# Optimization experiments

Measured on AMD Instinct MI355X. Metric: run time of the kernel, lower is better.

The kernel has to match this reference:

```python
import jax, jax.numpy as jnp
import numpy as np

B, N, DEG = 64, 512, 16        # graphs, nodes per graph, avg degree
C, HID = 10, 128               # input feat dim (== num_classes quirk), hidden
E = B * N * DEG                # total edges (fixed; pooling masks edges)


def _gcn(x, W, b, src, dst, emask, n):
    # PyG GCNConv: add self-loops, symmetric norm D^-1/2 (A+I) D^-1/2 (XW) + b
    h = x @ W
    deg = jax.ops.segment_sum(emask, dst, num_segments=n) + 1.0  # +1 self-loop
    dinv = jax.lax.rsqrt(deg)
    norm = dinv[src] * dinv[dst] * emask
    agg = jax.ops.segment_sum(h[src] * norm[:, None], dst, num_segments=n)
    return agg + h * (dinv * dinv)[:, None] + b  # self-loop term + bias


def _sag_pool(x, src, dst, emask, Wp, bp, n_per):
    # SAGPooling: score = tanh(GCN(x)); per-graph top-k (ratio=0.5); x' = x[perm]*score
    n = x.shape[0]
    score = jnp.tanh(_gcn(x, Wp, bp, src, dst, emask, n)[:, 0])
    k = n_per // 2
    vals, idx = jax.lax.top_k(score.reshape(B, n_per), k)  # [B,k]
    perm = (idx + (jnp.arange(B) * n_per)[:, None]).reshape(-1)
    xk = x[perm] * vals.reshape(-1)[:, None]
    # relabel edges; drop edges touching removed nodes via mask (fixed E)
    mapping = jnp.full((n,), -1, jnp.int32).at[perm].set(
        jnp.arange(B * k, dtype=jnp.int32))
    ns, nd = mapping[src], mapping[dst]
    nmask = emask * ((ns >= 0) & (nd >= 0)).astype(emask.dtype)
    return xk, jnp.maximum(ns, 0), jnp.maximum(nd, 0), nmask, k


def _readout(x, k):
    # global max pool || global mean pool (all kept nodes are real, no padding)
    xg = x.reshape(B, k, -1)
    return jnp.concatenate([xg.max(axis=1), xg.mean(axis=1)], axis=1)


def setup_inputs() -> dict:
    key = jax.random.key(0)
    ks = jax.random.split(key, 16)
    x = jax.random.normal(ks[0], (B * N, C), jnp.float32)
    off = jnp.repeat(jnp.arange(B, dtype=jnp.int32) * N, N * DEG)
    src = jax.random.randint(ks[1], (E,), 0, N, jnp.int32) + off
    dst = jax.random.randint(ks[2], (E,), 0, N, jnp.int32) + off
    p = lambda k, s: jax.random.normal(k, s, jnp.float32) * 0.05
    return {
        "x": x, "src": src, "dst": dst,
        "W1": p(ks[3], (C, HID)), "b1": jnp.zeros((HID,), jnp.float32),
        "W2": p(ks[4], (HID, HID)), "b2": jnp.zeros((HID,), jnp.float32),
        "W3": p(ks[5], (HID, HID)), "b3": jnp.zeros((HID,), jnp.float32),
        "Wp": p(ks[6], (HID, 1)), "bp": jnp.zeros((1,), jnp.float32),
        "L1W": p(ks[7], (2 * HID, HID)), "L1b": jnp.zeros((HID,), jnp.float32),
        "L2W": p(ks[8], (HID, HID // 2)), "L2b": jnp.zeros((HID // 2,), jnp.float32),
    }


def reference(x, src, dst, W1, b1, W2, b2, W3, b3, Wp, bp, L1W, L1b, L2W, L2b):
    emask = jnp.ones((E,), jnp.float32)
    h = jax.nn.relu(_gcn(x, W1, b1, src, dst, emask, B * N))
    h, src, dst, emask, k = _sag_pool(h, src, dst, emask, Wp, bp, N)
    x1 = _readout(h, k)
    h = jax.nn.relu(_gcn(h, W2, b2, src, dst, emask, B * k))
    h, src, dst, emask, k = _sag_pool(h, src, dst, emask, Wp, bp, k)
    x2 = _readout(h, k)
    h = jax.nn.relu(_gcn(h, W3, b3, src, dst, emask, B * k))
    h, src, dst, emask, k = _sag_pool(h, src, dst, emask, Wp, bp, k)
    x3 = _readout(h, k)
    z = x1 + x2 + x3
    z = jax.nn.relu(z @ L1W + L1b)
    # dropout inactive in eval mode
    z = jax.nn.relu(z @ L2W + L2b)
    return jax.nn.log_softmax(z, axis=1)
```

## Files before the change

### kernel.cpp

```cpp
#include <hip/hip_runtime.h>
#include <math.h>

#define BGR 64
#define N0 512
#define E_TOT (BGR*N0*16)
#define EPG 8192
#define HID 128
#define LOFF2 32768
#define LOFF3 49152

#define HSW(r,l) (((r)<<3) | (((l)+(r))&7))

__device__ __forceinline__ void bitonic_sort(float* sv, int* si, float v, int idx,
                                             int t, int nper, bool act){
  for (int kk = 2; kk <= nper; kk <<= 1){
    for (int jj = kk >> 1; jj > 0; jj >>= 1){
      if (jj >= 64){
        if (act){ sv[t] = v; si[t] = idx; }
        __syncthreads();
        if (act){
          int p = t ^ jj;
          float pv = sv[p]; int pi = si[p];
          bool amLower = (t & jj) == 0;
          bool dirDesc = (t & kk) == 0;
          bool betterMine = (v > pv) || (v == pv && idx < pi);
          if ((amLower == dirDesc) != betterMine){ v = pv; idx = pi; }
        }
        __syncthreads();
      } else if (act){
        float pv = __shfl_xor(v, jj);
        int   pi = __shfl_xor(idx, jj);
        bool amLower = (t & jj) == 0;
        bool dirDesc = (t & kk) == 0;
        bool betterMine = (v > pv) || (v == pv && idx < pi);
        if ((amLower == dirDesc) != betterMine){ v = pv; idx = pi; }
      }
    }
  }
  if (act){ sv[t] = v; si[t] = idx; }
  __syncthreads();
}

__device__ __forceinline__ void relabel_pre(
    int2* __restrict__ edges, int2* __restrict__ csr, const int* si,
    int* map_, int* sb, int* cur, float* dl, int* wsum,
    int* __restrict__ rowptr, int* __restrict__ cnt, float* __restrict__ dinv,
    const int2* epre,
    int t, int nper, int k, int gbase, int gbnew, int ebase, int loff){
  if (t < nper) map_[t] = -1;
  if (t < k) sb[t] = 0;
  __syncthreads();
  if (t < k) map_[si[t]] = t;
  __syncthreads();
  int2 ebuf[8];
  #pragma unroll
  for (int it = 0; it < 8; it++){
    int2 e = epre[it];
    int2 ne = make_int2(-1, 0);
    if (e.x >= 0){
      int ns = map_[e.x - gbase], nd = map_[e.y - gbase];
      if (ns >= 0 && nd >= 0){
        ne = make_int2(gbnew + ns, gbnew + nd);
        atomicAdd(&sb[nd], 1);
      }
    }
    ebuf[it] = ne;
    edges[ebase + it*1024 + t] = ne;
  }
  __syncthreads();
  int vdeg = (t < k) ? sb[t] : 0;
  int lane = t & 63, wid = t >> 6;
  int x = vdeg;
  #pragma unroll
  for (int off = 1; off < 64; off <<= 1){
    int y = __shfl_up(x, off);
    if (lane >= off) x += y;
  }
  if (t < k && lane == 63) wsum[wid] = x;
  __syncthreads();
  if (t < k){
    int prefix = 0;
    #pragma unroll
    for (int wj = 0; wj < 4; wj++) prefix += (wj < wid) ? wsum[wj] : 0;
    int excl = x + prefix - vdeg;
    rowptr[loff + gbnew + t] = ebase + excl;
    cnt[loff + gbnew + t] = vdeg;
    cur[t] = excl;
    float dv = rsqrtf((float)vdeg + 1.f);
    dl[t] = dv;
    dinv[loff + gbnew + t] = dv;
  }
  __syncthreads();
  #pragma unroll
  for (int it = 0; it < 8; it++){
    int2 e = ebuf[it];
    if (e.x >= 0){
      int sl = e.x - gbnew, dc = e.y - gbnew;
      int pos = atomicAdd(&cur[dc], 1);
      csr[ebase + pos] = make_int2(e.x, __float_as_int(dl[sl]*dl[dc]));
    }
  }
  __syncthreads();
}

__global__ __launch_bounds__(1024) void k_topo0(
    const int* __restrict__ s0, const int* __restrict__ d0,
    int2* __restrict__ edges, int* __restrict__ cnt, int* __restrict__ rowptr,
    float* __restrict__ dinv, int2* __restrict__ csr){
  __shared__ int   deg[512];
  __shared__ int   cur[512];
  __shared__ float dl[512];
  __shared__ int   wsum[8];
  int g = (blockIdx.x & 7)*8 + (blockIdx.x >> 3);
  int t = threadIdx.x;
  int gbase = g*N0, ebase = g*EPG;
  if (t < 512) deg[t] = 0;
  __syncthreads();
  int2 ebuf[8];
  #pragma unroll
  for (int it = 0; it < 8; it++){
    int i = ebase + it*1024 + t;
    int2 e = make_int2(s0[i], d0[i]);
    ebuf[it] = e;
    edges[i] = e;
    atomicAdd(&deg[e.y - gbase], 1);
  }
  __syncthreads();
  int vdeg = (t < 512) ? deg[t] : 0;
  int lane = t & 63, wid = t >> 6;
  int x = vdeg;
  #pragma unroll
  for (int off = 1; off < 64; off <<= 1){
    int y = __shfl_up(x, off);
    if (lane >= off) x += y;
  }
  if (t < 512 && lane == 63) wsum[wid] = x;
  __syncthreads();
  if (t < 512){
    int prefix = 0;
    #pragma unroll
    for (int wj = 0; wj < 8; wj++) prefix += (wj < wid) ? wsum[wj] : 0;
    int excl = x + prefix - vdeg;
    rowptr[gbase + t] = ebase + excl;
    cnt[gbase + t] = vdeg;
    cur[t] = excl;
    float dv = rsqrtf((float)vdeg + 1.f);
    dl[t] = dv;
    dinv[gbase + t] = dv;
  }
  __syncthreads();
  #pragma unroll
  for (int it = 0; it < 8; it++){
    int2 e = ebuf[it];
    int sl = e.x - gbase, dc = e.y - gbase;
    int pos = atomicAdd(&cur[dc], 1);
    csr[ebase + pos] = make_int2(e.x, __float_as_int(dl[sl]*dl[dc]));
  }
}

__global__ __launch_bounds__(512) void k_l1_fused(
    const float* __restrict__ x, const float* __restrict__ W1,
    const int2* __restrict__ csr, const int* __restrict__ rowptr,
    const int* __restrict__ cnt, const float* __restrict__ dinv,
    const float* __restrict__ b1, const float* __restrict__ Wp,
    float4* __restrict__ gout4, float* __restrict__ hp_part){
  extern __shared__ float hl[];
  int b = blockIdx.x;
  int xcd = b & 7, idx = b >> 3;
  int graph = xcd*8 + (idx >> 3);
  int sub = idx & 7;
  int qf = sub >> 1, half = sub & 1;
  int t = threadIdx.x;
  int gbase = graph*N0;
  int fp = t & 31;
  int f = qf*32 + fp;
  float wcol[10];
  #pragma unroll
  for (int k = 0; k < 10; k++) wcol[k] = W1[k*HID + f];
  for (int n = t >> 5; n < N0; n += 16){
    const float* xr = x + (gbase + n)*10;
    float acc = 0.f;
    #pragma unroll
    for (int k = 0; k < 10; k++) acc += xr[k]*wcol[k];
    hl[n*32 + ((((fp>>2)+n)&7)<<2) + (fp&3)] = acc;
  }
  __syncthreads();
  const float4* hl4 = (const float4*)hl;
  int l = t & 7, grp = t >> 3;
  float4 bb = ((const float4*)b1)[qf*8 + l];
  float4 wp = ((const float4*)Wp)[qf*8 + l];
  int n0 = half*256;
  for (int nl = n0 + grp; nl < n0 + 256; nl += 64){
    int node = gbase + nl;
    int start = rowptr[node], c = cnt[node];
    float4 acc = make_float4(0.f,0.f,0.f,0.f);
    int j = 0;
    for (; j + 4 <= c; j += 4){
      int2 e0 = csr[start+j],   e1 = csr[start+j+1];
      int2 e2 = csr[start+j+2], e3 = csr[start+j+3];
      float4 h0 = hl4[HSW(e0.x - gbase, l)];
      float4 h1 = hl4[HSW(e1.x - gbase, l)];
      float4 h2 = hl4[HSW(e2.x - gbase, l)];
      float4 h3 = hl4[HSW(e3.x - gbase, l)];
      float w0 = __int_as_float(e0.y), w1 = __int_as_float(e1.y);
      float w2 = __int_as_float(e2.y), w3 = __int_as_float(e3.y);
      acc.x += w0*h0.x + w1*h1.x + w2*h2.x + w3*h3.x;
      acc.y += w0*h0.y + w1*h1.y + w2*h2.y + w3*h3.y;
      acc.z += w0*h0.z + w1*h1.z + w2*h2.z + w3*h3.z;
      acc.w += w0*h0.w + w1*h1.w + w2*h2.w + w3*h3.w;
    }
    for (; j < c; j++){
      int2 e = csr[start + j];
      float wgt = __int_as_float(e.y);
      float4 hv = hl4[HSW(e.x - gbase, l)];
      acc.x += wgt*hv.x; acc.y += wgt*hv.y; acc.z += wgt*hv.z; acc.w += wgt*hv.w;
    }
    float di = dinv[node], dd = di*di;
    float4 hs = hl4[HSW(nl, l)];
    float4 v;
    v.x = fmaxf(acc.x + hs.x*dd + bb.x, 0.f);
    v.y = fmaxf(acc.y + hs.y*dd + bb.y, 0.f);
    v.z = fmaxf(acc.z + hs.z*dd + bb.z, 0.f);
    v.w = fmaxf(acc.w + hs.w*dd + bb.w, 0.f);
    gout4[node*32 + qf*8 + l] = v;
    float contrib = v.x*wp.x + v.y*wp.y + v.z*wp.z + v.w*wp.w;
    #pragma unroll
    for (int off = 4; off; off >>= 1) contrib += __shfl_down(contrib, off, 8);
    if (l == 0) hp_part[qf*32768 + node] = contrib;
  }
}

__global__ __launch_bounds__(1024) void k_mega1(
    const float4* __restrict__ gout4, const float* __restrict__ hppt,
    int2* __restrict__ csr, int* __restrict__ rowptr, int* __restrict__ cnt,
    float* __restrict__ dinv, const float* __restrict__ bp,
    int2* __restrict__ edges, int* __restrict__ sig, float* __restrict__ svg,
    float* __restrict__ z){
  __shared__ float sv[512];
  __shared__ int   si[512];
  __shared__ float hpl[512];
  __shared__ union UA {
    float spart[1024];
    struct { float4 pmx[32][32]; float4 psm[32][32]; } ro;
    struct { int map_[512]; int sb[512]; int cur[256]; } rl;
  } u;
  __shared__ float dl[256];
  __shared__ int   wsum[4];
  int g = (blockIdx.x & 7)*8 + (blockIdx.x >> 3);
  int t = threadIdx.x;
  int gbase = g*N0, ebase = g*EPG, gb2 = g*256;
  float bp0 = bp[0];
  int2 epre[8];
  #pragma unroll
  for (int it = 0; it < 8; it++) epre[it] = edges[ebase + it*1024 + t];
  if (t < 512){
    int node = gbase + t;
    hpl[t] = hppt[node] + hppt[32768+node] + hppt[65536+node] + hppt[98304+node];
  }
  __syncthreads();
  {
    int n = t & 511, p = t >> 9;
    int start = rowptr[gbase + n], c = cnt[gbase + n];
    int lo = (c*p) >> 1, hi = (c*(p+1)) >> 1;
    float a = 0.f;
    for (int j = lo; j < hi; j++){
      int2 e = csr[start + j];
      a += __int_as_float(e.y)*hpl[e.x - gbase];
    }
    u.spart[t] = a;
  }
  __syncthreads();
  float v = 0.f; int idx = t;
  if (t < 512){
    float a = u.spart[t] + u.spart[t + 512];
    float di = dinv[gbase + t];
    v = tanhf(a + hpl[t]*di*di + bp0);
  }
  __syncthreads();
  bitonic_sort(sv, si, v, idx, t, 512, t < 512);
  if (t < 256){ sig[g*512 + t] = si[t]; svg[g*512 + t] = sv[t]; }
  int l = t & 31, j0 = t >> 5;
  {
    float4 mx = make_float4(-INFINITY,-INFINITY,-INFINITY,-INFINITY);
    float4 sm = make_float4(0.f,0.f,0.f,0.f);
    for (int j = j0; j < 256; j += 32){
      float val = sv[j]; int row = si[j];
      float4 hv = gout4[(gbase + row)*32 + l];
      float4 o = make_float4(hv.x*val, hv.y*val, hv.z*val, hv.w*val);
      mx.x = fmaxf(mx.x, o.x); mx.y = fmaxf(mx.y, o.y);
      mx.z = fmaxf(mx.z, o.z); mx.w = fmaxf(mx.w, o.w);
      sm.x += o.x; sm.y += o.y; sm.z += o.z; sm.w += o.w;
    }
    u.ro.pmx[j0][l] = mx; u.ro.psm[j0][l] = sm;
  }
  __syncthreads();
  if (t < 32){
    float4 M = u.ro.pmx[0][t], S = u.ro.psm[0][t];
    #pragma unroll
    for (int q = 1; q < 32; q++){
      float4 m2 = u.ro.pmx[q][t], s2 = u.ro.psm[q][t];
      M.x = fmaxf(M.x, m2.x); M.y = fmaxf(M.y, m2.y);
      M.z = fmaxf(M.z, m2.z); M.w = fmaxf(M.w, m2.w);
      S.x += s2.x; S.y += s2.y; S.z += s2.z; S.w += s2.w;
    }
    float ki = 1.f/256.f;
    float* zp = z + g*256;
    zp[t*4+0] = M.x; zp[t*4+1] = M.y; zp[t*4+2] = M.z; zp[t*4+3] = M.w;
    zp[128+t*4+0] = S.x*ki; zp[128+t*4+1] = S.y*ki;
    zp[128+t*4+2] = S.z*ki; zp[128+t*4+3] = S.w*ki;
  }
  __syncthreads();
  relabel_pre(edges, csr, si, u.rl.map_, u.rl.sb, u.rl.cur, dl, wsum,
              rowptr, cnt, dinv, epre, t, 512, 256, gbase, gb2, ebase, LOFF2);
}

__global__ __launch_bounds__(512) void k_lvl2(
    const float4* __restrict__ gout4,
    const int* __restrict__ sig, const float* __restrict__ svg,
    const float* __restrict__ W2, const float* __restrict__ b2,
    const float* __restrict__ Wp,
    const int2* __restrict__ csr, const int* __restrict__ rowptr,
    const int* __restrict__ cnt, const float* __restrict__ dinv,
    float4* __restrict__ g2out4, float* __restrict__ hp2p){
  __shared__ float hL[256*32];
  int b = blockIdx.x;
  int jb = b & 63, s8 = b >> 6;
  int s = s8 >> 1, half = s8 & 1;
  int g = (jb & 7)*8 + (jb >> 3);
  int t = threadIdx.x;
  int gbase = g*N0, gb2 = g*256;
  float4* hL4 = (float4*)hL;
  {
    int f4 = t & 7, rg = t >> 3;
    int rbase = rg*4;
    const float* Wb = W2 + s*32 + f4*4;
    int ri[4]; float rv[4];
    #pragma unroll
    for (int q = 0; q < 4; q++){
      ri[q] = sig[g*512 + rbase + q];
      rv[q] = svg[g*512 + rbase + q];
    }
    float4 acc[4];
    #pragma unroll
    for (int q = 0; q < 4; q++) acc[q] = make_float4(0.f,0.f,0.f,0.f);
    for (int i = 0; i < HID; i += 4){
      float4 w0 = *(const float4*)(Wb + (i+0)*HID);
      float4 w1 = *(const float4*)(Wb + (i+1)*HID);
      float4 w2 = *(const float4*)(Wb + (i+2)*HID);
      float4 w3 = *(const float4*)(Wb + (i+3)*HID);
      #pragma unroll
      for (int q = 0; q < 4; q++){
        float4 xv = gout4[(gbase + ri[q])*32 + (i>>2)];
        float vx = xv.x*rv[q], vy = xv.y*rv[q], vz = xv.z*rv[q], vw = xv.w*rv[q];
        acc[q].x += vx*w0.x + vy*w1.x + vz*w2.x + vw*w3.x;
        acc[q].y += vx*w0.y + vy*w1.y + vz*w2.y + vw*w3.y;
        acc[q].z += vx*w0.z + vy*w1.z + vz*w2.z + vw*w3.z;
        acc[q].w += vx*w0.w + vy*w1.w + vz*w2.w + vw*w3.w;
      }
    }
    #pragma unroll
    for (int q = 0; q < 4; q++) hL4[HSW(rbase+q, f4)] = acc[q];
  }
  __syncthreads();
  int l = t & 7, grpn = t >> 3;
  float4 bb = ((const float4*)b2)[s*8 + l];
  float4 wp = ((const float4*)Wp)[s*8 + l];
  for (int it = 0; it < 2; it++){
    int n = half*128 + it*64 + grpn;
    int node = gb2 + n;
    int start = rowptr[LOFF2 + node], c = cnt[LOFF2 + node];
    float4 acc = make_float4(0.f,0.f,0.f,0.f);
    int j = 0;
    for (; j + 4 <= c; j += 4){
      int2 e0 = csr[start+j],   e1 = csr[start+j+1];
      int2 e2 = csr[start+j+2], e3 = csr[start+j+3];
      float4 h0 = hL4[HSW(e0.x - gb2, l)];
      float4 h1 = hL4[HSW(e1.x - gb2, l)];
      float4 h2 = hL4[HSW(e2.x - gb2, l)];
      float4 h3 = hL4[HSW(e3.x - gb2, l)];
      float w0 = __int_as_float(e0.y), w1 = __int_as_float(e1.y);
      float w2 = __int_as_float(e2.y), w3 = __int_as_float(e3.y);
      acc.x += w0*h0.x + w1*h1.x + w2*h2.x + w3*h3.x;
      acc.y += w0*h0.y + w1*h1.y + w2*h2.y + w3*h3.y;
      acc.z += w0*h0.z + w1*h1.z + w2*h2.z + w3*h3.z;
      acc.w += w0*h0.w + w1*h1.w + w2*h2.w + w3*h3.w;
    }
    for (; j < c; j++){
      int2 e = csr[start + j];
      float wgt = __int_as_float(e.y);
      float4 hv = hL4[HSW(e.x - gb2, l)];
      acc.x += wgt*hv.x; acc.y += wgt*hv.y; acc.z += wgt*hv.z; acc.w += wgt*hv.w;
    }
    float di = dinv[LOFF2 + node], dd = di*di;
    float4 hs = hL4[HSW(n, l)];
    float4 v;
    v.x = fmaxf(acc.x + hs.x*dd + bb.x, 0.f);
    v.y = fmaxf(acc.y + hs.y*dd + bb.y, 0.f);
    v.z = fmaxf(acc.z + hs.z*dd + bb.z, 0.f);
    v.w = fmaxf(acc.w + hs.w*dd + bb.w, 0.f);
    g2out4[node*32 + s*8 + l] = v;
    float contrib = v.x*wp.x + v.y*wp.y + v.z*wp.z + v.w*wp.w;
    #pragma unroll
    for (int off = 4; off; off >>= 1) contrib += __shfl_down(contrib, off, 8);
    if (l == 0) hp2p[s*16384 + node] = contrib;
  }
}

__global__ __launch_bounds__(1024) void k_mega2(
    const float4* __restrict__ g2out4, const float* __restrict__ hp2p,
    int2* __restrict__ csr, int* __restrict__ rowptr, int* __restrict__ cnt,
    float* __restrict__ dinv, const float* __restrict__ bp,
    int2* __restrict__ edges, int* __restrict__ sig, float* __restrict__ svg,
    float* __restrict__ z){
  __shared__ float sv[256];
  __shared__ int   si[256];
  __shared__ float hpl[256];
  __shared__ union UB {
    float spart[1024];
    struct { float4 pmx[32][32]; float4 psm[32][32]; } ro;
    struct { int map_[256]; int sb[128]; int cur[128]; } rl;
  } u;
  __shared__ float dl[128];
  __shared__ int   wsum[4];
  int g = (blockIdx.x & 7)*8 + (blockIdx.x >> 3);
  int t = threadIdx.x;
  int gb2 = g*256, gb3 = g*128, ebase = g*EPG;
  float bp0 = bp[0];
  int2 epre[8];
  #pragma unroll
  for (int it = 0; it < 8; it++) epre[it] = edges[ebase + it*1024 + t];
  if (t < 256){
    int node = gb2 + t;
    hpl[t] = hp2p[node] + hp2p[16384+node] + hp2p[32768+node] + hp2p[49152+node];
  }
  __syncthreads();
  {
    int n = t & 255, p = t >> 8;
    int start = rowptr[LOFF2 + gb2 + n], c = cnt[LOFF2 + gb2 + n];
    int lo = (c*p) >> 2, hi = (c*(p+1)) >> 2;
    float a = 0.f;
    for (int j = lo; j < hi; j++){
      int2 e = csr[start + j];
      a += __int_as_float(e.y)*hpl[e.x - gb2];
    }
    u.spart[t] = a;
  }
  __syncthreads();
  float v = 0.f; int idx = t;
  if (t < 256){
    float a = u.spart[t] + u.spart[t+256] + u.spart[t+512] + u.spart[t+768];
    float di = dinv[LOFF2 + gb2 + t];
    v = tanhf(a + hpl[t]*di*di + bp0);
  }
  __syncthreads();
  bitonic_sort(sv, si, v, idx, t, 256, t < 256);
  if (t < 128){ sig[g*512 + t] = si[t]; svg[g*512 + t] = sv[t]; }
  int l = t & 31, j0 = t >> 5;
  {
    float4 mx = make_float4(-INFINITY,-INFINITY,-INFINITY,-INFINITY);
    float4 sm = make_float4(0.f,0.f,0.f,0.f);
    for (int j = j0; j < 128; j += 32){
      float val = sv[j]; int row = si[j];
      float4 hv = g2out4[(gb2 + row)*32 + l];
      float4 o = make_float4(hv.x*val, hv.y*val, hv.z*val, hv.w*val);
      mx.x = fmaxf(mx.x, o.x); mx.y = fmaxf(mx.y, o.y);
      mx.z = fmaxf(mx.z, o.z); mx.w = fmaxf(mx.w, o.w);
      sm.x += o.x; sm.y += o.y; sm.z += o.z; sm.w += o.w;
    }
    u.ro.pmx[j0][l] = mx; u.ro.psm[j0][l] = sm;
  }
  __syncthreads();
  if (t < 32){
    float4 M = u.ro.pmx[0][t], S = u.ro.psm[0][t];
    #pragma unroll
    for (int q = 1; q < 32; q++){
      float4 m2 = u.ro.pmx[q][t], s2 = u.ro.psm[q][t];
      M.x = fmaxf(M.x, m2.x); M.y = fmaxf(M.y, m2.y);
      M.z = fmaxf(M.z, m2.z); M.w = fmaxf(M.w, m2.w);
      S.x += s2.x; S.y += s2.y; S.z += s2.z; S.w += s2.w;
    }
    float ki = 1.f/128.f;
    float* zp = z + g*256;
    zp[t*4+0] += M.x; zp[t*4+1] += M.y; zp[t*4+2] += M.z; zp[t*4+3] += M.w;
    zp[128+t*4+0] += S.x*ki; zp[128+t*4+1] += S.y*ki;
    zp[128+t*4+2] += S.z*ki; zp[128+t*4+3] += S.w*ki;
  }
  __syncthreads();
  relabel_pre(edges, csr, si, u.rl.map_, u.rl.sb, u.rl.cur, dl, wsum,
              rowptr, cnt, dinv, epre, t, 256, 128, gb2, gb3, ebase, LOFF3);
}

__global__ __launch_bounds__(512) void k_lvl3(
    const float4* __restrict__ g2out4,
    const int* __restrict__ sig, const float* __restrict__ svg,
    const float* __restrict__ W3, const float* __restrict__ b3,
    const float* __restrict__ Wp,
    const int2* __restrict__ csr, const int* __restrict__ rowptr,
    const int* __restrict__ cnt, const float* __restrict__ dinv,
    float4* __restrict__ g3out4, float* __restrict__ hp3p){
  __shared__ float hL[128*32];
  int b = blockIdx.x;
  int jb = b & 63, s8 = b >> 6;
  int s = s8 >> 1, half = s8 & 1;
  int g = (jb & 7)*8 + (jb >> 3);
  int t = threadIdx.x;
  int gb2 = g*256, gb3 = g*128;
  float4* hL4 = (float4*)hL;
  {
    int f4 = t & 7, rg = t >> 3;
    int rbase = rg*2;
    const float* Wb = W3 + s*32 + f4*4;
    int ri[2]; float rv[2];
    #pragma unroll
    for (int q = 0; q < 2; q++){
      ri[q] = sig[g*512 + rbase + q];
      rv[q] = svg[g*512 + rbase + q];
    }
    float4 acc[2];
    #pragma unroll
    for (int q = 0; q < 2; q++) acc[q] = make_float4(0.f,0.f,0.f,0.f);
    for (int i = 0; i < HID; i += 4){
      float4 w0 = *(const float4*)(Wb + (i+0)*HID);
      float4 w1 = *(const float4*)(Wb + (i+1)*HID);
      float4 w2 = *(const float4*)(Wb + (i+2)*HID);
      float4 w3 = *(const float4*)(Wb + (i+3)*HID);
      #pragma unroll
      for (int q = 0; q < 2; q++){
        float4 xv = g2out4[(gb2 + ri[q])*32 + (i>>2)];
        float vx = xv.x*rv[q], vy = xv.y*rv[q], vz = xv.z*rv[q], vw = xv.w*rv[q];
        acc[q].x += vx*w0.x + vy*w1.x + vz*w2.x + vw*w3.x;
        acc[q].y += vx*w0.y + vy*w1.y + vz*w2.y + vw*w3.y;
        acc[q].z += vx*w0.z + vy*w1.z + vz*w2.z + vw*w3.z;
        acc[q].w += vx*w0.w + vy*w1.w + vz*w2.w + vw*w3.w;
      }
    }
    #pragma unroll
    for (int q = 0; q < 2; q++) hL4[HSW(rbase+q, f4)] = acc[q];
  }
  __syncthreads();
  int l = t & 7, grpn = t >> 3;
  float4 bb = ((const float4*)b3)[s*8 + l];
  float4 wp = ((const float4*)Wp)[s*8 + l];
  {
    int n = half*64 + grpn;
    int node = gb3 + n;
    int start = rowptr[LOFF3 + node], c = cnt[LOFF3 + node];
    float4 acc = make_float4(0.f,0.f,0.f,0.f);
    int j = 0;
    for (; j + 4 <= c; j += 4){
      int2 e0 = csr[start+j],   e1 = csr[start+j+1];
      int2 e2 = csr[start+j+2], e3 = csr[start+j+3];
      float4 h0 = hL4[HSW(e0.x - gb3, l)];
      float4 h1 = hL4[HSW(e1.x - gb3, l)];
      float4 h2 = hL4[HSW(e2.x - gb3, l)];
      float4 h3 = hL4[HSW(e3.x - gb3, l)];
      float w0 = __int_as_float(e0.y), w1 = __int_as_float(e1.y);
      float w2 = __int_as_float(e2.y), w3 = __int_as_float(e3.y);
      acc.x += w0*h0.x + w1*h1.x + w2*h2.x + w3*h3.x;
      acc.y += w0*h0.y + w1*h1.y + w2*h2.y + w3*h3.y;
      acc.z += w0*h0.z + w1*h1.z + w2*h2.z + w3*h3.z;
      acc.w += w0*h0.w + w1*h1.w + w2*h2.w + w3*h3.w;
    }
    for (; j < c; j++){
      int2 e = csr[start + j];
      float wgt = __int_as_float(e.y);
      float4 hv = hL4[HSW(e.x - gb3, l)];
      acc.x += wgt*hv.x; acc.y += wgt*hv.y; acc.z += wgt*hv.z; acc.w += wgt*hv.w;
    }
    float di = dinv[LOFF3 + node], dd = di*di;
    float4 hs = hL4[HSW(n, l)];
    float4 v;
    v.x = fmaxf(acc.x + hs.x*dd + bb.x, 0.f);
    v.y = fmaxf(acc.y + hs.y*dd + bb.y, 0.f);
    v.z = fmaxf(acc.z + hs.z*dd + bb.z, 0.f);
    v.w = fmaxf(acc.w + hs.w*dd + bb.w, 0.f);
    g3out4[node*32 + s*8 + l] = v;
    float contrib = v.x*wp.x + v.y*wp.y + v.z*wp.z + v.w*wp.w;
    #pragma unroll
    for (int off = 4; off; off >>= 1) contrib += __shfl_down(contrib, off, 8);
    if (l == 0) hp3p[s*8192 + node] = contrib;
  }
}

__global__ __launch_bounds__(1024) void k_mega3(
    const float4* __restrict__ g3out4, const float* __restrict__ hp3p,
    const int2* __restrict__ csr, const int* __restrict__ rowptr,
    const int* __restrict__ cnt, const float* __restrict__ dinv,
    const float* __restrict__ bp, float* __restrict__ z,
    const float* __restrict__ L1W, const float* __restrict__ L1b,
    const float* __restrict__ L2W, const float* __restrict__ L2b,
    float* __restrict__ out){
  __shared__ float sv[128];
  __shared__ int   si[128];
  __shared__ float hpl[128];
  __shared__ union UC {
    float spart[1024];
    struct { float4 pmx[32][32]; float4 psm[32][32]; } ro;
  } u;
  __shared__ float zr[256];
  __shared__ float h1l[128];
  __shared__ float h2l[64];
  __shared__ float red[2];
  int g = (blockIdx.x & 7)*8 + (blockIdx.x >> 3);
  int t = threadIdx.x;
  int gb3 = g*128;
  float bp0 = bp[0];
  if (t < 128){
    int node = gb3 + t;
    hpl[t] = hp3p[node] + hp3p[8192+node] + hp3p[16384+node] + hp3p[24576+node];
  }
  __syncthreads();
  {
    int n = t & 127, p = t >> 7;
    int start = rowptr[LOFF3 + gb3 + n], c = cnt[LOFF3 + gb3 + n];
    int lo = (c*p) >> 3, hi = (c*(p+1)) >> 3;
    float a = 0.f;
    for (int j = lo; j < hi; j++){
      int2 e = csr[start + j];
      a += __int_as_float(e.y)*hpl[e.x - gb3];
    }
    u.spart[t] = a;
  }
  __syncthreads();
  float v = 0.f; int idx = t;
  if (t < 128){
    float a = 0.f;
    #pragma unroll
    for (int pp = 0; pp < 8; pp++) a += u.spart[t + pp*128];
    float di = dinv[LOFF3 + gb3 + t];
    v = tanhf(a + hpl[t]*di*di + bp0);
  }
  __syncthreads();
  bitonic_sort(sv, si, v, idx, t, 128, t < 128);
  int l = t & 31, j0 = t >> 5;
  {
    float4 mx = make_float4(-INFINITY,-INFINITY,-INFINITY,-INFINITY);
    float4 sm = make_float4(0.f,0.f,0.f,0.f);
    for (int j = j0; j < 64; j += 32){
      float val = sv[j]; int row = si[j];
      float4 hv = g3out4[(gb3 + row)*32 + l];
      float4 o = make_float4(hv.x*val, hv.y*val, hv.z*val, hv.w*val);
      mx.x = fmaxf(mx.x, o.x); mx.y = fmaxf(mx.y, o.y);
      mx.z = fmaxf(mx.z, o.z); mx.w = fmaxf(mx.w, o.w);
      sm.x += o.x; sm.y += o.y; sm.z += o.z; sm.w += o.w;
    }
    u.ro.pmx[j0][l] = mx; u.ro.psm[j0][l] = sm;
  }
  __syncthreads();
  if (t < 32){
    float4 M = u.ro.pmx[0][t], S = u.ro.psm[0][t];
    #pragma unroll
    for (int q = 1; q < 32; q++){
      float4 m2 = u.ro.pmx[q][t], s2 = u.ro.psm[q][t];
      M.x = fmaxf(M.x, m2.x); M.y = fmaxf(M.y, m2.y);
      M.z = fmaxf(M.z, m2.z); M.w = fmaxf(M.w, m2.w);
      S.x += s2.x; S.y += s2.y; S.z += s2.z; S.w += s2.w;
    }
    float ki = 1.f/64.f;
    float* zp = z + g*256;
    zr[t*4+0] = zp[t*4+0] + M.x; zr[t*4+1] = zp[t*4+1] + M.y;
    zr[t*4+2] = zp[t*4+2] + M.z; zr[t*4+3] = zp[t*4+3] + M.w;
    zr[128+t*4+0] = zp[128+t*4+0] + S.x*ki;
    zr[128+t*4+1] = zp[128+t*4+1] + S.y*ki;
    zr[128+t*4+2] = zp[128+t*4+2] + S.z*ki;
    zr[128+t*4+3] = zp[128+t*4+3] + S.w*ki;
  }
  __syncthreads();
  if (t < 128){
    float a = L1b[t];
    for (int i = 0; i < 256; i++) a += zr[i]*L1W[i*128 + t];
    h1l[t] = fmaxf(a, 0.f);
  }
  __syncthreads();
  if (t < 64){
    float a = L2b[t];
    for (int i = 0; i < 128; i++) a += h1l[i]*L2W[i*64 + t];
    h2l[t] = fmaxf(a, 0.f);
  }
  __syncthreads();
  if (t == 0){
    float mxv = -INFINITY;
    for (int i = 0; i < 64; i++) mxv = fmaxf(mxv, h2l[i]);
    float s = 0.f;
    for (int i = 0; i < 64; i++) s += expf(h2l[i] - mxv);
    red[0] = mxv; red[1] = logf(s);
  }
  __syncthreads();
  if (t < 64) out[g*64 + t] = h2l[t] - red[0] - red[1];
}

extern "C" void kernel_launch(void* const* d_in, const int* in_sizes, int n_in,
                              void* d_out, int out_size, void* d_ws, size_t ws_size,
                              hipStream_t stream){
  (void)in_sizes; (void)n_in; (void)out_size; (void)ws_size;
  const float* x0  = (const float*)d_in[0];
  const int*   s0  = (const int*)  d_in[1];
  const int*   d0  = (const int*)  d_in[2];
  const float* W1  = (const float*)d_in[3];  const float* b1 = (const float*)d_in[4];
  const float* W2  = (const float*)d_in[5];  const float* b2 = (const float*)d_in[6];
  const float* W3  = (const float*)d_in[7];  const float* b3 = (const float*)d_in[8];
  const float* Wp  = (const float*)d_in[9];  const float* bp = (const float*)d_in[10];
  const float* L1W = (const float*)d_in[11]; const float* L1b = (const float*)d_in[12];
  const float* L2W = (const float*)d_in[13]; const float* L2b = (const float*)d_in[14];
  float* out = (float*)d_out;

  float* w = (float*)d_ws;
  float* gout1 = w; w += 32768*HID;
  float* gout2 = w; w += 16384*HID;
  float* gout3 = w; w += 8192*HID;
  float* dinvv = w; w += 65536;
  float* hppt  = w; w += 4*32768;
  float* hp2p  = w; w += 4*16384;
  float* hp3p  = w; w += 4*8192;
  float* z     = w; w += BGR*256;
  float* svg   = w; w += 32768;
  int* sig     = (int*)w; w += 32768;
  int* cnt     = (int*)w; w += 65536;
  int* rowptr  = (int*)w; w += 65536;
  int2* edges  = (int2*)w; w += 2*E_TOT;
  int2* csr    = (int2*)w; w += 2*E_TOT;

  k_topo0<<<BGR, 1024, 0, stream>>>(s0, d0, edges, cnt, rowptr, dinvv, csr);
  k_l1_fused<<<512, 512, 65536, stream>>>(x0, W1, csr, rowptr, cnt, dinvv,
                                          b1, Wp, (float4*)gout1, hppt);
  k_mega1<<<BGR, 1024, 0, stream>>>((const float4*)gout1, hppt, csr, rowptr,
                                    cnt, dinvv, bp, edges, sig, svg, z);
  k_lvl2<<<8*BGR, 512, 0, stream>>>((const float4*)gout1, sig, svg, W2, b2, Wp,
                                    csr, rowptr, cnt, dinvv,
                                    (float4*)gout2, hp2p);
  k_mega2<<<BGR, 1024, 0, stream>>>((const float4*)gout2, hp2p, csr, rowptr,
                                    cnt, dinvv, bp, edges, sig, svg, z);
  k_lvl3<<<8*BGR, 512, 0, stream>>>((const float4*)gout2, sig, svg, W3, b3, Wp,
                                    csr, rowptr, cnt, dinvv,
                                    (float4*)gout3, hp3p);
  k_mega3<<<BGR, 1024, 0, stream>>>((const float4*)gout3, hp3p, csr, rowptr,
                                    cnt, dinvv, bp, z,
                                    L1W, L1b, L2W, L2b, out);
}
```

Baseline: 242.5 us.

## Stage gathered pooled rows in shared memory and drop half-split in lvl2/lvl3

The lvl2 and lvl3 kernels now stage the gathered, score-scaled input rows into a swizzled shared-memory tile in 64-row chunks with coalesced float4 loads. Each thread then computes one output row-slice from shared memory instead of issuing strided global gathers per input element. The node-half split is removed, so each block handles all nodes of its graph for one feature slice and the grid halves. This means the transform is no longer computed twice per half. The cost is fewer blocks, more shared memory per block, and extra barriers per chunk.

Result: slower. 370.2 us (+52.6%).

```diff
diff --git a/kernel.cpp b/kernel.cpp
--- a/kernel.cpp
+++ b/kernel.cpp
@@ -10,6 +10,7 @@
 #define LOFF3 49152
 
 #define HSW(r,l) (((r)<<3) | (((l)+(r))&7))
+#define XST(r,q) (((r)<<5) | (((q)+(r))&31))
 
 __device__ __forceinline__ void bitonic_sort(float* sv, int* si, float v, int idx,
                                              int t, int nper, bool act){
@@ -322,51 +323,54 @@
     const int2* __restrict__ csr, const int* __restrict__ rowptr,
     const int* __restrict__ cnt, const float* __restrict__ dinv,
     float4* __restrict__ g2out4, float* __restrict__ hp2p){
+  __shared__ float xst[64*HID];
   __shared__ float hL[256*32];
   int b = blockIdx.x;
-  int jb = b & 63, s8 = b >> 6;
-  int s = s8 >> 1, half = s8 & 1;
+  int jb = b & 63, s = b >> 6;
   int g = (jb & 7)*8 + (jb >> 3);
   int t = threadIdx.x;
   int gbase = g*N0, gb2 = g*256;
   float4* hL4 = (float4*)hL;
-  {
-    int f4 = t & 7, rg = t >> 3;
-    int rbase = rg*4;
-    const float* Wb = W2 + s*32 + f4*4;
-    int ri[4]; float rv[4];
-    #pragma unroll
-    for (int q = 0; q < 4; q++){
-      ri[q] = sig[g*512 + rbase + q];
-      rv[q] = svg[g*512 + rbase + q];
-    }
-    float4 acc[4];
-    #pragma unroll
-    for (int q = 0; q < 4; q++) acc[q] = make_float4(0.f,0.f,0.f,0.f);
-    for (int i = 0; i < HID; i += 4){
-      float4 w0 = *(const float4*)(Wb + (i+0)*HID);
-      float4 w1 = *(const float4*)(Wb + (i+1)*HID);
-      float4 w2 = *(const float4*)(Wb + (i+2)*HID);
-      float4 w3 = *(const float4*)(Wb + (i+3)*HID);
+  float4* xst4 = (float4*)xst;
+  int f4 = t & 7, rg = t >> 3;
+  const float* Wb = W2 + s*32 + f4*4;
+  for (int c0 = 0; c0 < 256; c0 += 64){
+    {
+      int row = t >> 3;
+      int q0 = (t & 7)*4;
+      int pr = c0 + row;
+      int ri = sig[g*512 + pr];
+      float rv = svg[g*512 + pr];
+      const float4* src = gout4 + (gbase + ri)*32;
       #pragma unroll
       for (int q = 0; q < 4; q++){
-        float4 xv = gout4[(gbase + ri[q])*32 + (i>>2)];
-        float vx = xv.x*rv[q], vy = xv.y*rv[q], vz = xv.z*rv[q], vw = xv.w*rv[q];
-        acc[q].x += vx*w0.x + vy*w1.x + vz*w2.x + vw*w3.x;
-        acc[q].y += vx*w0.y + vy*w1.y + vz*w2.y + vw*w3.y;
-        acc[q].z += vx*w0.z + vy*w1.z + vz*w2.z + vw*w3.z;
-        acc[q].w += vx*w0.w + vy*w1.w + vz*w2.w + vw*w3.w;
+        float4 a = src[q0 + q];
+        xst4[XST(row, q0 + q)] = make_float4(a.x*rv, a.y*rv, a.z*rv, a.w*rv);
       }
     }
-    #pragma unroll
-    for (int q = 0; q < 4; q++) hL4[HSW(rbase+q, f4)] = acc[q];
-  }
-  __syncthreads();
+    __syncthreads();
+    {
+      float4 acc = make_float4(0.f,0.f,0.f,0.f);
+      for (int i = 0; i < HID; i += 4){
+        float4 w0 = *(const float4*)(Wb + (i+0)*HID);
+        float4 w1 = *(const float4*)(Wb + (i+1)*HID);
+        float4 w2 = *(const float4*)(Wb + (i+2)*HID);
+        float4 w3 = *(const float4*)(Wb + (i+3)*HID);
+        float4 xv = xst4[XST(rg, i>>2)];
+        acc.x += xv.x*w0.x + xv.y*w1.x + xv.z*w2.x + xv.w*w3.x;
+        acc.y += xv.x*w0.y + xv.y*w1.y + xv.z*w2.y + xv.w*w3.y;
+        acc.z += xv.x*w0.z + xv.y*w1.z + xv.z*w2.z + xv.w*w3.z;
+        acc.w += xv.x*w0.w + xv.y*w1.w + xv.z*w2.w + xv.w*w3.w;
+      }
+      hL4[HSW(c0 + rg, f4)] = acc;
+    }
+    __syncthreads();
+  }
   int l = t & 7, grpn = t >> 3;
   float4 bb = ((const float4*)b2)[s*8 + l];
   float4 wp = ((const float4*)Wp)[s*8 + l];
-  for (int it = 0; it < 2; it++){
-    int n = half*128 + it*64 + grpn;
+  for (int it = 0; it < 4; it++){
+    int n = it*64 + grpn;
     int node = gb2 + n;
     int start = rowptr[LOFF2 + node], c = cnt[LOFF2 + node];
     float4 acc = make_float4(0.f,0.f,0.f,0.f);
@@ -498,51 +502,54 @@
     const int2* __restrict__ csr, const int* __restrict__ rowptr,
     const int* __restrict__ cnt, const float* __restrict__ dinv,
     float4* __restrict__ g3out4, float* __restrict__ hp3p){
+  __shared__ float xst[64*HID];
   __shared__ float hL[128*32];
   int b = blockIdx.x;
-  int jb = b & 63, s8 = b >> 6;
-  int s = s8 >> 1, half = s8 & 1;
+  int jb = b & 63, s = b >> 6;
   int g = (jb & 7)*8 + (jb >> 3);
   int t = threadIdx.x;
   int gb2 = g*256, gb3 = g*128;
   float4* hL4 = (float4*)hL;
-  {
-    int f4 = t & 7, rg = t >> 3;
-    int rbase = rg*2;
-    const float* Wb = W3 + s*32 + f4*4;
-    int ri[2]; float rv[2];
-    #pragma unroll
-    for (int q = 0; q < 2; q++){
-      ri[q] = sig[g*512 + rbase + q];
-      rv[q] = svg[g*512 + rbase + q];
-    }
-    float4 acc[2];
-    #pragma unroll
-    for (int q = 0; q < 2; q++) acc[q] = make_float4(0.f,0.f,0.f,0.f);
-    for (int i = 0; i < HID; i += 4){
-      float4 w0 = *(const float4*)(Wb + (i+0)*HID);
-      float4 w1 = *(const float4*)(Wb + (i+1)*HID);
-      float4 w2 = *(const float4*)(Wb + (i+2)*HID);
-      float4 w3 = *(const float4*)(Wb + (i+3)*HID);
+  float4* xst4 = (float4*)xst;
+  int f4 = t & 7, rg = t >> 3;
+  const float* Wb = W3 + s*32 + f4*4;
+  for (int c0 = 0; c0 < 128; c0 += 64){
+    {
+      int row = t >> 3;
+      int q0 = (t & 7)*4;
+      int pr = c0 + row;
+      int ri = sig[g*512 + pr];
+      float rv = svg[g*512 + pr];
+      const float4* src = g2out4 + (gb2 + ri)*32;
       #pragma unroll
-      for (int q = 0; q < 2; q++){
-        float4 xv = g2out4[(gb2 + ri[q])*32 + (i>>2)];
-        float vx = xv.x*rv[q], vy = xv.y*rv[q], vz = xv.z*rv[q], vw = xv.w*rv[q];
-        acc[q].x += vx*w0.x + vy*w1.x + vz*w2.x + vw*w3.x;
-        acc[q].y += vx*w0.y + vy*w1.y + vz*w2.y + vw*w3.y;
-        acc[q].z += vx*w0.z + vy*w1.z + vz*w2.z + vw*w3.z;
-        acc[q].w += vx*w0.w + vy*w1.w + vz*w2.w + vw*w3.w;
+      for (int q = 0; q < 4; q++){
+        float4 a = src[q0 + q];
+        xst4[XST(row, q0 + q)] = make_float4(a.x*rv, a.y*rv, a.z*rv, a.w*rv);
       }
     }
-    #pragma unroll
-    for (int q = 0; q < 2; q++) hL4[HSW(rbase+q, f4)] = acc[q];
-  }
-  __syncthreads();
+    __syncthreads();
+    {
+      float4 acc = make_float4(0.f,0.f,0.f,0.f);
+      for (int i = 0; i < HID; i += 4){
+        float4 w0 = *(const float4*)(Wb + (i+0)*HID);
+        float4 w1 = *(const float4*)(Wb + (i+1)*HID);
+        float4 w2 = *(const float4*)(Wb + (i+2)*HID);
+        float4 w3 = *(const float4*)(Wb + (i+3)*HID);
+        float4 xv = xst4[XST(rg, i>>2)];
+        acc.x += xv.x*w0.x + xv.y*w1.x + xv.z*w2.x + xv.w*w3.x;
+        acc.y += xv.x*w0.y + xv.y*w1.y + xv.z*w2.y + xv.w*w3.y;
+        acc.z += xv.x*w0.z + xv.y*w1.z + xv.z*w2.z + xv.w*w3.z;
+        acc.w += xv.x*w0.w + xv.y*w1.w + xv.z*w2.w + xv.w*w3.w;
+      }
+      hL4[HSW(c0 + rg, f4)] = acc;
+    }
+    __syncthreads();
+  }
   int l = t & 7, grpn = t >> 3;
   float4 bb = ((const float4*)b3)[s*8 + l];
   float4 wp = ((const float4*)Wp)[s*8 + l];
-  {
-    int n = half*64 + grpn;
+  for (int it = 0; it < 2; it++){
+    int n = it*64 + grpn;
     int node = gb3 + n;
     int start = rowptr[LOFF3 + node], c = cnt[LOFF3 + node];
     float4 acc = make_float4(0.f,0.f,0.f,0.f);
@@ -725,12 +732,12 @@
                                           b1, Wp, (float4*)gout1, hppt);
   k_mega1<<<BGR, 1024, 0, stream>>>((const float4*)gout1, hppt, csr, rowptr,
                                     cnt, dinvv, bp, edges, sig, svg, z);
-  k_lvl2<<<8*BGR, 512, 0, stream>>>((const float4*)gout1, sig, svg, W2, b2, Wp,
+  k_lvl2<<<4*BGR, 512, 0, stream>>>((const float4*)gout1, sig, svg, W2, b2, Wp,
                                     csr, rowptr, cnt, dinvv,
                                     (float4*)gout2, hp2p);
   k_mega2<<<BGR, 1024, 0, stream>>>((const float4*)gout2, hp2p, csr, rowptr,
                                     cnt, dinvv, bp, edges, sig, svg, z);
-  k_lvl3<<<8*BGR, 512, 0, stream>>>((const float4*)gout2, sig, svg, W3, b3, Wp,
+  k_lvl3<<<4*BGR, 512, 0, stream>>>((const float4*)gout2, sig, svg, W3, b3, Wp,
                                     csr, rowptr, cnt, dinvv,
                                     (float4*)gout3, hp3p);
   k_mega3<<<BGR, 1024, 0, stream>>>((const float4*)gout3, hp3p, csr, rowptr,
```
